# Optimization experiments

Hardware: AMD Instinct MI355X
Metric: run time of the kernel (lower is better)

The kernel has to match this reference:

```python
import jax, jax.numpy as jnp
import numpy as np

# Static multi-level feature-map shapes (H, W) per level.
SPATIAL_SHAPES = np.array([[92, 160], [46, 80], [23, 40], [12, 20]], dtype=np.int32)
NUM_HEADS = 8
NUM_LEVELS = 4
NUM_POINTS = 4      # sampling points per head per level (num_all_points)
NUM_Z = 4           # num_Z_anchors; NUM_POINTS % NUM_Z == 0
EMBED = 256
HEAD_DIM = EMBED // NUM_HEADS


def setup_inputs() -> dict:
    key = jax.random.key(0)
    ks = jax.random.split(key, 10)
    bs, nq = 2, 10000
    nv = int((SPATIAL_SHAPES[:, 0] * SPATIAL_SHAPES[:, 1]).sum())  # 19560
    query = jax.random.normal(ks[0], (bs, nq, EMBED), jnp.float32)
    value = jax.random.normal(ks[1], (bs, nv, EMBED), jnp.float32)
    query_pos = jax.random.normal(ks[2], (bs, nq, EMBED), jnp.float32)
    reference_points = jax.random.uniform(ks[3], (bs, nq, NUM_Z, 2), jnp.float32)
    W_val = jax.random.normal(ks[4], (EMBED, EMBED), jnp.float32) / jnp.sqrt(EMBED)
    b_val = jnp.zeros((EMBED,), jnp.float32)
    W_off = jax.random.normal(ks[5], (EMBED, NUM_HEADS * NUM_LEVELS * NUM_POINTS * 2), jnp.float32) * 0.01
    b_off = jax.random.normal(ks[6], (NUM_HEADS * NUM_LEVELS * NUM_POINTS * 2,), jnp.float32) * 0.5
    W_attn = jax.random.normal(ks[7], (EMBED, NUM_HEADS * NUM_LEVELS * NUM_POINTS), jnp.float32) * 0.02
    b_attn = jnp.zeros((NUM_HEADS * NUM_LEVELS * NUM_POINTS,), jnp.float32)
    spatial_shapes = jnp.asarray(SPATIAL_SHAPES)
    return {
        'query': query, 'value': value, 'query_pos': query_pos,
        'reference_points': reference_points,
        'W_val': W_val, 'b_val': b_val, 'W_off': W_off, 'b_off': b_off,
        'W_attn': W_attn, 'b_attn': b_attn, 'spatial_shapes': spatial_shapes,
    }


def _bilinear(v, x, y, H, W):
    """grid_sample(mode='bilinear', padding_mode='zeros', align_corners=False).

    v: (bs, H, W, heads, d); x, y: (bs, nq, heads, P) pixel coords.
    Returns (bs, nq, heads, P, d).
    """
    x0 = jnp.floor(x)
    y0 = jnp.floor(y)
    wx1 = x - x0
    wy1 = y - y0
    wx0 = 1.0 - wx1
    wy0 = 1.0 - wy1
    x0i = x0.astype(jnp.int32)
    y0i = y0.astype(jnp.int32)
    b = jnp.arange(v.shape[0])[:, None, None, None]
    h = jnp.arange(v.shape[3])[None, None, :, None]

    def gather(yi, xi):
        valid = (yi >= 0) & (yi < H) & (xi >= 0) & (xi < W)
        yc = jnp.clip(yi, 0, H - 1)
        xc = jnp.clip(xi, 0, W - 1)
        g = v[b, yc, xc, h]  # (bs, nq, heads, P, d)
        return g * valid[..., None].astype(v.dtype)

    return (gather(y0i, x0i) * (wy0 * wx0)[..., None]
            + gather(y0i, x0i + 1) * (wy0 * wx1)[..., None]
            + gather(y0i + 1, x0i) * (wy1 * wx0)[..., None]
            + gather(y0i + 1, x0i + 1) * (wy1 * wx1)[..., None])


def reference(query, value, query_pos, reference_points, W_val, b_val,
              W_off, b_off, W_attn, b_attn, spatial_shapes):
    bs, nq, _ = query.shape
    q = query + query_pos
    # value projection -> per-head values
    v = (value @ W_val + b_val).reshape(bs, -1, NUM_HEADS, HEAD_DIM)
    # sampling offsets and attention weights from query
    off = (q @ W_off + b_off).reshape(bs, nq, NUM_HEADS, NUM_LEVELS, NUM_POINTS, 2)
    attn = (q @ W_attn + b_attn).reshape(bs, nq, NUM_HEADS, NUM_LEVELS * NUM_POINTS)
    attn = jax.nn.softmax(attn, axis=-1).reshape(bs, nq, NUM_HEADS, NUM_LEVELS, NUM_POINTS)
    # normalize offsets by (w, h) of each level
    norm = jnp.stack([spatial_shapes[:, 1], spatial_shapes[:, 0]], -1).astype(q.dtype)  # (L, 2)
    off = off / norm[None, None, None, :, None, :]
    # fold Z-anchor reference points in, matching the shape[-1]==2 branch
    off = off.reshape(bs, nq, NUM_HEADS, NUM_LEVELS, NUM_POINTS // NUM_Z, NUM_Z, 2)
    loc = reference_points[:, :, None, None, None, :, :] + off
    loc = loc.reshape(bs, nq, NUM_HEADS, NUM_LEVELS, NUM_POINTS, 2)
    grid = 2.0 * loc - 1.0  # grid_sample convention

    start = 0
    sampled = []
    for lvl in range(NUM_LEVELS):
        H, W = int(SPATIAL_SHAPES[lvl, 0]), int(SPATIAL_SHAPES[lvl, 1])
        vl = v[:, start:start + H * W].reshape(bs, H, W, NUM_HEADS, HEAD_DIM)
        start += H * W
        # align_corners=False pixel coords
        x = ((grid[:, :, :, lvl, :, 0] + 1.0) * W - 1.0) * 0.5
        y = ((grid[:, :, :, lvl, :, 1] + 1.0) * H - 1.0) * 0.5
        sampled.append(_bilinear(vl, x, y, H, W))
    samp = jnp.stack(sampled, axis=3)  # (bs, nq, heads, L, P, d)
    out = (samp * attn[..., None]).sum(axis=(3, 4))  # (bs, nq, heads, d)
    return out.reshape(bs, nq, NUM_HEADS * HEAD_DIM)
```

## Files before the change

### kernel.cpp

```cpp
#include <hip/hip_runtime.h>

#define NQ 10000
#define BS 2
#define NV 19560
#define NH 8
#define HD 32
#define EMB 256

typedef __attribute__((ext_vector_type(8))) short bf16x8;
typedef __attribute__((ext_vector_type(4))) float f32x4;
typedef __attribute__((ext_vector_type(4))) short s16x4;

__device__ __forceinline__ unsigned short f2bf(float x) {
    unsigned u = __float_as_uint(x);
    u += 0x7FFFu + ((u >> 16) & 1u);
    return (unsigned short)(u >> 16);
}

__global__ __launch_bounds__(256) void convert_W(
    const float* __restrict__ Wv, const float* __restrict__ Wo,
    const float* __restrict__ Wa, const float* __restrict__ bv,
    const float* __restrict__ bo, const float* __restrict__ ba,
    ushort* __restrict__ Bt, float* __restrict__ bias) {
    int n = blockIdx.x;
    int k = threadIdx.x;
    float x;
    if (n < 256)       x = Wv[k * 256 + n];
    else if (n < 512)  x = Wo[k * 256 + (n - 256)];
    else               x = Wa[k * 128 + (n - 512)];
    Bt[n * 256 + k] = f2bf(x);
    if (k == 0)
        bias[n] = (n < 256) ? bv[n] : (n < 512) ? bo[n - 256] : ba[n - 512];
}

__global__ __launch_bounds__(256) void gemm_fused(
    const float* __restrict__ value, const float* __restrict__ query,
    const float* __restrict__ qpos, const ushort* __restrict__ Bt,
    const float* __restrict__ bias,
    ushort* __restrict__ Cv, float* __restrict__ C0, float* __restrict__ C1)
{
    __shared__ short As[64][40], Bhs[128][40];

    const int tid = threadIdx.x;
    const int bid = blockIdx.x;
    bool isval; int mblk, npan;
    if (bid < 1224) { isval = true;  mblk = bid >> 1; npan = bid & 1; }
    else { int q = bid - 1224; isval = false; mblk = q / 3; npan = q % 3; }

    const int M  = isval ? (BS * NV) : (BS * NQ);
    const int m0 = mblk * 64;
    const int n0 = npan * 128;
    const int nbase = (isval ? 0 : 256) + n0;

    const float* A = isval ? value : query;

    const int arow = tid >> 2;
    const int acol = (tid & 3) * 8;
    const bool aval = (m0 + arow) < M;
    const float* Ap  = A    + (size_t)(m0 + arow) * 256 + acol;
    const float* A2p = qpos + (size_t)(m0 + arow) * 256 + acol;
    const int brow = tid >> 1;
    const int bcol = (tid & 1) * 16;
    const ushort* Bp = Bt + (size_t)(nbase + brow) * 256 + bcol;

    const int lane = tid & 63, wave = tid >> 6;
    const int wrow = (wave >> 1) * 32, wcol = (wave & 1) * 64;
    const int lr = lane & 15, quad = lane >> 4, lk = quad * 8;

    f32x4 acc[2][4] = {};

    for (int k0 = 0; k0 < 256; k0 += 32) {
        #pragma unroll
        for (int g = 0; g < 2; g++) {
            f32x4 v = {};
            if (aval) {
                v = *(const f32x4*)(Ap + k0 + g * 4);
                if (!isval) v += *(const f32x4*)(A2p + k0 + g * 4);
            }
            s16x4 hh;
            #pragma unroll
            for (int e = 0; e < 4; e++) hh[e] = (short)f2bf(v[e]);
            *(s16x4*)&As[arow][acol + g * 4] = hh;
        }
        *(bf16x8*)&Bhs[brow][bcol]     = *(const bf16x8*)(Bp + k0);
        *(bf16x8*)&Bhs[brow][bcol + 8] = *(const bf16x8*)(Bp + k0 + 8);
        __syncthreads();

        bf16x8 af[2], bhf[4];
        #pragma unroll
        for (int i = 0; i < 2; i++)
            af[i] = *(const bf16x8*)&As[wrow + i * 16 + lr][lk];
        #pragma unroll
        for (int j = 0; j < 4; j++)
            bhf[j] = *(const bf16x8*)&Bhs[wcol + j * 16 + lr][lk];
        #pragma unroll
        for (int i = 0; i < 2; i++)
            #pragma unroll
            for (int j = 0; j < 4; j++)
                acc[i][j] = __builtin_amdgcn_mfma_f32_16x16x32_bf16(af[i], bhf[j], acc[i][j], 0, 0, 0);
        __syncthreads();
    }

    #pragma unroll
    for (int j = 0; j < 4; j++) {
        int cc = wcol + j * 16 + lr;
        int col = n0 + cc;
        float bb = bias[nbase + cc];
        #pragma unroll
        for (int i = 0; i < 2; i++) {
            int gmb = m0 + wrow + i * 16 + quad * 4;
            #pragma unroll
            for (int r = 0; r < 4; r++) {
                int gm = gmb + r;
                if (gm < M) {
                    float val = acc[i][j][r] + bb;
                    if (isval) {
                        int h = col >> 5, d = col & 31;
                        int b = (gm >= NV) ? 1 : 0;
                        int pix = gm - b * NV;
                        Cv[((size_t)(b * 8 + h) * NV + pix) * 32 + d] = f2bf(val);
                    } else {
                        if (col < 256) C0[(size_t)gm * 256 + col] = val;
                        else           C1[(size_t)gm * 128 + (col - 256)] = val;
                    }
                }
            }
        }
    }
}

__global__ __launch_bounds__(256) void sample6(
    const ushort* __restrict__ v, const float* __restrict__ off,
    const float* __restrict__ attn, const float* __restrict__ refp,
    float* __restrict__ out)
{
    __shared__ int   s_off[64][66];
    __shared__ float s_w[64][66];

    const int bq0 = blockIdx.x * 8;
    const int t = threadIdx.x;

    #pragma unroll
    for (int rep = 0; rep < 4; rep++) {
        const int id = rep * 256 + t;
        const int g = id >> 4;
        const int qi = g >> 3, h = g & 7;
        const int bq = bq0 + qi;
        const int b = (bq >= NQ) ? 1 : 0;
        const int i = id & 15;
        const int l = i >> 2, p = i & 3;

        float logit = attn[(size_t)bq * 128 + h * 16 + i];
        float mx = logit;
        #pragma unroll
        for (int m = 1; m < 16; m <<= 1) mx = fmaxf(mx, __shfl_xor(mx, m, 16));
        float e = __expf(logit - mx);
        float s = e;
        #pragma unroll
        for (int m = 1; m < 16; m <<= 1) s += __shfl_xor(s, m, 16);
        float w = e / s;

        const float Wf[4] = {160.f, 80.f, 40.f, 20.f};
        const float Hf[4] = {92.f, 46.f, 23.f, 12.f};
        const int   Wi[4] = {160, 80, 40, 20};
        const int   Hi[4] = {92, 46, 23, 12};
        const int   st[4] = {0, 14720, 18400, 19320};

        float ox = off[(size_t)bq * 256 + h * 32 + l * 8 + p * 2];
        float oy = off[(size_t)bq * 256 + h * 32 + l * 8 + p * 2 + 1];
        float rx = refp[(size_t)bq * 8 + p * 2];
        float ry = refp[(size_t)bq * 8 + p * 2 + 1];
        float x = rx * Wf[l] + ox - 0.5f;
        float y = ry * Hf[l] + oy - 0.5f;
        float x0f = floorf(x), y0f = floorf(y);
        float wx1 = x - x0f, wy1 = y - y0f;
        float wx0 = 1.f - wx1, wy0 = 1.f - wy1;
        int x0 = (int)x0f, y0 = (int)y0f;
        const int W = Wi[l], H = Hi[l];
        float mx0 = ((unsigned)x0       < (unsigned)W) ? 1.f : 0.f;
        float mx1 = ((unsigned)(x0 + 1) < (unsigned)W) ? 1.f : 0.f;
        float my0 = ((unsigned)y0       < (unsigned)H) ? 1.f : 0.f;
        float my1 = ((unsigned)(y0 + 1) < (unsigned)H) ? 1.f : 0.f;
        int xc0 = min(max(x0, 0), W - 1);
        int xc1 = min(max(x0 + 1, 0), W - 1);
        int yc0 = min(max(y0, 0), H - 1);
        int yc1 = min(max(y0 + 1, 0), H - 1);
        int base = ((b * 8 + h) * NV + st[l]) * 32;
        s_off[g][i * 4 + 0] = base + (yc0 * W + xc0) * 32;
        s_off[g][i * 4 + 1] = base + (yc0 * W + xc1) * 32;
        s_off[g][i * 4 + 2] = base + (yc1 * W + xc0) * 32;
        s_off[g][i * 4 + 3] = base + (yc1 * W + xc1) * 32;
        s_w[g][i * 4 + 0] = w * wy0 * wx0 * my0 * mx0;
        s_w[g][i * 4 + 1] = w * wy0 * wx1 * my0 * mx1;
        s_w[g][i * 4 + 2] = w * wy1 * wx0 * my1 * mx0;
        s_w[g][i * 4 + 3] = w * wy1 * wx1 * my1 * mx1;
    }
    __syncthreads();

    const int g  = t >> 2;
    const int c4 = t & 3;
    const int qi = g >> 3, h = g & 7;
    const int bq = bq0 + qi;
    const int d8 = c4 * 8;

    float a0=0.f,a1=0.f,a2=0.f,a3=0.f,a4=0.f,a5=0.f,a6=0.f,a7=0.f;
    #pragma unroll
    for (int i = 0; i < 16; i += 2) {
        int o[8]; float wgt[8];
        #pragma unroll
        for (int pp = 0; pp < 2; pp++)
            #pragma unroll
            for (int c = 0; c < 4; c++) {
                o[pp * 4 + c]   = s_off[g][(i + pp) * 4 + c];
                wgt[pp * 4 + c] = s_w[g][(i + pp) * 4 + c];
            }
        uint4 u[8];
        #pragma unroll
        for (int j = 0; j < 8; j++)
            u[j] = *(const uint4*)(v + o[j] + d8);
        #pragma unroll
        for (int j = 0; j < 8; j++) {
            float w = wgt[j];
            a0 += w * __uint_as_float(u[j].x << 16);
            a1 += w * __uint_as_float(u[j].x & 0xffff0000u);
            a2 += w * __uint_as_float(u[j].y << 16);
            a3 += w * __uint_as_float(u[j].y & 0xffff0000u);
            a4 += w * __uint_as_float(u[j].z << 16);
            a5 += w * __uint_as_float(u[j].z & 0xffff0000u);
            a6 += w * __uint_as_float(u[j].w << 16);
            a7 += w * __uint_as_float(u[j].w & 0xffff0000u);
        }
    }
    float* op = out + (size_t)bq * 256 + h * 32 + d8;
    f32x4 r0 = {a0, a1, a2, a3};
    f32x4 r1 = {a4, a5, a6, a7};
    *(f32x4*)op       = r0;
    *(f32x4*)(op + 4) = r1;
}

extern "C" void kernel_launch(void* const* d_in, const int* in_sizes, int n_in,
                              void* d_out, int out_size, void* d_ws, size_t ws_size,
                              hipStream_t stream) {
    const float* query     = (const float*)d_in[0];
    const float* value     = (const float*)d_in[1];
    const float* query_pos = (const float*)d_in[2];
    const float* refp      = (const float*)d_in[3];
    const float* W_val     = (const float*)d_in[4];
    const float* b_val     = (const float*)d_in[5];
    const float* W_off     = (const float*)d_in[6];
    const float* b_off     = (const float*)d_in[7];
    const float* W_attn    = (const float*)d_in[8];
    const float* b_attn    = (const float*)d_in[9];
    float* out = (float*)d_out;

    char* w = (char*)d_ws;
    float*  off    = (float*)w;   w += 20480000;
    float*  attn   = (float*)w;   w += 10240000;
    ushort* vp_bf  = (ushort*)w;  w += 20029440;
    ushort* Bt     = (ushort*)w;  w += 327680;
    float*  bias_c = (float*)w;   w += 2560;

    convert_W<<<640, 256, 0, stream>>>(W_val, W_off, W_attn, b_val, b_off, b_attn,
                                       Bt, bias_c);

    gemm_fused<<<1224 + 939, 256, 0, stream>>>(value, query, query_pos, Bt, bias_c,
                                               vp_bf, off, attn);

    sample6<<<BS * NQ / 8, 256, 0, stream>>>(vp_bf, off, attn, refp, out);
}
```

Measured before the change: 222.3 us.

## Prefetch GEMM K-tiles into registers and shrink sampling blocks to one wave

The fused GEMM now uses a 64-wide K tile and loads the next tile's A and B data into registers while MFMAs run on the current LDS tile. This halves the loop trips and hides global-load latency behind compute. Separately, the sampling kernel drops from 256-thread blocks covering 8 queries to 64-thread blocks covering 2 queries, which cuts per-block LDS and allows finer scheduling. The costs are more registers and LDS per GEMM block, which may lower occupancy, and many more small sampling blocks to launch.

Result: slower. 230.1 us (+3.5%).

```diff
diff --git a/kernel.cpp b/kernel.cpp
--- a/kernel.cpp
+++ b/kernel.cpp
@@ -39,7 +39,7 @@
     const float* __restrict__ bias,
     ushort* __restrict__ Cv, float* __restrict__ C0, float* __restrict__ C1)
 {
-    __shared__ short As[64][40], Bhs[128][40];
+    __shared__ short As[64][72], Bhs[128][72];
 
     const int tid = threadIdx.x;
     const int bid = blockIdx.x;
@@ -55,49 +55,89 @@
     const float* A = isval ? value : query;
 
     const int arow = tid >> 2;
-    const int acol = (tid & 3) * 8;
+    const int acol = (tid & 3) * 16;
     const bool aval = (m0 + arow) < M;
     const float* Ap  = A    + (size_t)(m0 + arow) * 256 + acol;
     const float* A2p = qpos + (size_t)(m0 + arow) * 256 + acol;
     const int brow = tid >> 1;
-    const int bcol = (tid & 1) * 16;
+    const int bcol = (tid & 1) * 32;
     const ushort* Bp = Bt + (size_t)(nbase + brow) * 256 + bcol;
 
     const int lane = tid & 63, wave = tid >> 6;
     const int wrow = (wave >> 1) * 32, wcol = (wave & 1) * 64;
-    const int lr = lane & 15, quad = lane >> 4, lk = quad * 8;
+    const int lr = lane & 15, quad = lane >> 4;
+
+    f32x4 aR[4]; bf16x8 bR[4];
+
+    #pragma unroll
+    for (int g = 0; g < 4; g++) {
+        f32x4 v = {};
+        if (aval) {
+            v = *(const f32x4*)(Ap + g * 4);
+            if (!isval) v += *(const f32x4*)(A2p + g * 4);
+        }
+        aR[g] = v;
+    }
+    #pragma unroll
+    for (int c = 0; c < 4; c++) bR[c] = *(const bf16x8*)(Bp + c * 8);
+    #pragma unroll
+    for (int g = 0; g < 4; g++) {
+        s16x4 hh;
+        #pragma unroll
+        for (int e = 0; e < 4; e++) hh[e] = (short)f2bf(aR[g][e]);
+        *(s16x4*)&As[arow][acol + g * 4] = hh;
+    }
+    #pragma unroll
+    for (int c = 0; c < 4; c++) *(bf16x8*)&Bhs[brow][bcol + c * 8] = bR[c];
+    __syncthreads();
 
     f32x4 acc[2][4] = {};
 
-    for (int k0 = 0; k0 < 256; k0 += 32) {
-        #pragma unroll
-        for (int g = 0; g < 2; g++) {
-            f32x4 v = {};
-            if (aval) {
-                v = *(const f32x4*)(Ap + k0 + g * 4);
-                if (!isval) v += *(const f32x4*)(A2p + k0 + g * 4);
+    #pragma unroll
+    for (int k0 = 0; k0 < 256; k0 += 64) {
+        if (k0 < 192) {
+            #pragma unroll
+            for (int g = 0; g < 4; g++) {
+                f32x4 v = {};
+                if (aval) {
+                    v = *(const f32x4*)(Ap + k0 + 64 + g * 4);
+                    if (!isval) v += *(const f32x4*)(A2p + k0 + 64 + g * 4);
+                }
+                aR[g] = v;
             }
-            s16x4 hh;
-            #pragma unroll
-            for (int e = 0; e < 4; e++) hh[e] = (short)f2bf(v[e]);
-            *(s16x4*)&As[arow][acol + g * 4] = hh;
-        }
-        *(bf16x8*)&Bhs[brow][bcol]     = *(const bf16x8*)(Bp + k0);
-        *(bf16x8*)&Bhs[brow][bcol + 8] = *(const bf16x8*)(Bp + k0 + 8);
+            #pragma unroll
+            for (int c = 0; c < 4; c++)
+                bR[c] = *(const bf16x8*)(Bp + k0 + 64 + c * 8);
+        }
+        #pragma unroll
+        for (int sub = 0; sub < 2; sub++) {
+            const int lk = sub * 32 + quad * 8;
+            bf16x8 af[2], bhf[4];
+            #pragma unroll
+            for (int i = 0; i < 2; i++)
+                af[i] = *(const bf16x8*)&As[wrow + i * 16 + lr][lk];
+            #pragma unroll
+            for (int j = 0; j < 4; j++)
+                bhf[j] = *(const bf16x8*)&Bhs[wcol + j * 16 + lr][lk];
+            #pragma unroll
+            for (int i = 0; i < 2; i++)
+                #pragma unroll
+                for (int j = 0; j < 4; j++)
+                    acc[i][j] = __builtin_amdgcn_mfma_f32_16x16x32_bf16(af[i], bhf[j], acc[i][j], 0, 0, 0);
+        }
         __syncthreads();
-
-        bf16x8 af[2], bhf[4];
-        #pragma unroll
-        for (int i = 0; i < 2; i++)
-            af[i] = *(const bf16x8*)&As[wrow + i * 16 + lr][lk];
-        #pragma unroll
-        for (int j = 0; j < 4; j++)
-            bhf[j] = *(const bf16x8*)&Bhs[wcol + j * 16 + lr][lk];
-        #pragma unroll
-        for (int i = 0; i < 2; i++)
-            #pragma unroll
-            for (int j = 0; j < 4; j++)
-                acc[i][j] = __builtin_amdgcn_mfma_f32_16x16x32_bf16(af[i], bhf[j], acc[i][j], 0, 0, 0);
+        if (k0 < 192) {
+            #pragma unroll
+            for (int g = 0; g < 4; g++) {
+                s16x4 hh;
+                #pragma unroll
+                for (int e = 0; e < 4; e++) hh[e] = (short)f2bf(aR[g][e]);
+                *(s16x4*)&As[arow][acol + g * 4] = hh;
+            }
+            #pragma unroll
+            for (int c = 0; c < 4; c++)
+                *(bf16x8*)&Bhs[brow][bcol + c * 8] = bR[c];
+        }
         __syncthreads();
     }
 
@@ -129,20 +169,20 @@
     }
 }
 
-__global__ __launch_bounds__(256) void sample6(
+__global__ __launch_bounds__(64) void sample7(
     const ushort* __restrict__ v, const float* __restrict__ off,
     const float* __restrict__ attn, const float* __restrict__ refp,
     float* __restrict__ out)
 {
-    __shared__ int   s_off[64][66];
-    __shared__ float s_w[64][66];
-
-    const int bq0 = blockIdx.x * 8;
+    __shared__ int   s_off[16][66];
+    __shared__ float s_w[16][66];
+
+    const int bq0 = blockIdx.x * 2;
     const int t = threadIdx.x;
 
     #pragma unroll
     for (int rep = 0; rep < 4; rep++) {
-        const int id = rep * 256 + t;
+        const int id = rep * 64 + t;
         const int g = id >> 4;
         const int qi = g >> 3, h = g & 7;
         const int bq = bq0 + qi;
@@ -266,5 +306,5 @@
     gemm_fused<<<1224 + 939, 256, 0, stream>>>(value, query, query_pos, Bt, bias_c,
                                                vp_bf, off, attn);
 
-    sample6<<<BS * NQ / 8, 256, 0, stream>>>(vp_bf, off, attn, refp, out);
-}
+    sample7<<<BS * NQ / 2, 64, 0, stream>>>(vp_bf, off, attn, refp, out);
+}
```
